# Performance work log

Measured on AMD Instinct MI355X. Metric: run time of the kernel, lower is better.

Reference implementation:

```python
import jax, jax.numpy as jnp
import numpy as np

CH, H, N, N_SSM, SEQ_L = 1, 1024, 64, 1024, 2048


def setup_inputs() -> dict:
    key = jax.random.key(0)
    ks = jax.random.split(key, 5)
    return {
        "C_ri": jax.random.normal(ks[0], (CH, H, N, 2), dtype=jnp.float32),
        "log_dt": jax.random.normal(ks[1], (H,), dtype=jnp.float32),
        "B_ri": jax.random.normal(ks[2], (N_SSM, N, 2), dtype=jnp.float32),
        "inv_A_real": jax.random.normal(ks[3], (N_SSM, N), dtype=jnp.float32),
        "A_imag": jax.random.normal(ks[4], (N_SSM, N), dtype=jnp.float32),
        "L": SEQ_L,
    }


def _kernel(C_ri, log_dt, B_ri, inv_A_real, A_imag, L):
    # Reconstruct complex params from real views (torch view_as_complex)
    C = C_ri[..., 0] + 1j * C_ri[..., 1]        # (CH, H, N) complex64
    B = B_ri[..., 0] + 1j * B_ri[..., 1]        # (n_ssm, N)
    A = -jnp.exp(inv_A_real) + 1j * A_imag      # (n_ssm, N), Re(A) < 0

    rep = log_dt.shape[0] // inv_A_real.shape[0]  # H // n_ssm
    B = jnp.tile(B, (rep, 1))                   # 't n -> (v t) n' : (H, N)
    A = jnp.tile(A, (rep, 1))                   # (H, N)

    dt = jnp.exp(log_dt)                        # (H,), rate = 1.0
    dtA = A * dt[:, None]                       # (H, N)

    # C <- B * C * dt / (1 - dtA/2)   (bilinear discretization of input/output)
    Ct = (B[None] * C) / (1.0 - dtA / 2) * dt[:, None]   # (CH, H, N)
    dA = (1.0 + dtA / 2) / (1.0 - dtA / 2)      # (H, N), |dA| < 1
    dA_log = jnp.log(dA)                        # (H, N)

    # log-Vandermonde: K[c,h,l] = 2 * Re( sum_n Ct[c,h,n] * exp(dA_log[h,n] * l) )
    l = jnp.arange(L, dtype=jnp.float32)
    V = jnp.exp(dA_log[:, :, None] * l)         # (H, N, L) complex
    K = 2.0 * jnp.einsum('chn,hnl->chl', Ct, V).real  # (CH, H, L)
    return K


def reference(C_ri, log_dt, B_ri, inv_A_real, A_imag, L):
    # state=None path: returns (K, K_state=None); we return K
    return _kernel(C_ri, log_dt, B_ri, inv_A_real, A_imag, L)
```

## Files before the change

kernel.cpp:

```cpp
#include <hip/hip_runtime.h>
#include <math.h>

#define CH 1
#define H 1024
#define NN 64
#define N_SSM 1024
#define SEQ_L 2048
#define TPB 128
#define LPT 16

typedef float v2f __attribute__((ext_vector_type(2)));

__device__ __forceinline__ v2f lo2(const float4 f) { v2f r; r.x = f.x; r.y = f.y; return r; }
__device__ __forceinline__ v2f hi2(const float4 f) { v2f r; r.x = f.z; r.y = f.w; return r; }

__global__ __launch_bounds__(TPB) void sskd_kernel(
    const float* __restrict__ C_ri, const float* __restrict__ log_dt,
    const float* __restrict__ B_ri, const float* __restrict__ inv_A_real,
    const float* __restrict__ A_imag, float* __restrict__ out)
{
    const int h   = blockIdx.x;
    const int tid = threadIdx.x;

    __shared__ __align__(16) float4 sU1[8][33], sV1[8][33], sU8[8][33], sV8[8][33];
    __shared__ __align__(16) float4 sT[16][33];
    __shared__ __align__(16) float4 sPQ[32];
    __shared__ double sW8r[NN], sW8i[NN], sW16r[NN], sW16i[NN], sW256r[NN], sW256i[NN];
    __shared__ double sCtr[NN], sCti[NN], sCdr[NN], sCdi[NN];

    if (tid < NN) {
        const int n = tid;
        const double dt = exp((double)log_dt[h]);
        const double Ar = -exp((double)inv_A_real[h * NN + n]);
        const double Ai = (double)A_imag[h * NN + n];
        const double hr = 0.5 * Ar * dt, hi = 0.5 * Ai * dt;
        const double den_r = 1.0 - hr, den_i = -hi;
        const double num_r = 1.0 + hr, num_i = hi;
        const double inv_den = 1.0 / (den_r * den_r + den_i * den_i);
        const double dAr = (num_r * den_r + num_i * den_i) * inv_den;
        const double dAi = (num_i * den_r - num_r * den_i) * inv_den;
        const int    bh = h % N_SSM;
        const double Br = B_ri[(bh * NN + n) * 2 + 0];
        const double Bi = B_ri[(bh * NN + n) * 2 + 1];
        const double Cr = C_ri[(h * NN + n) * 2 + 0];
        const double Ci = C_ri[(h * NN + n) * 2 + 1];
        const double BCr = Br * Cr - Bi * Ci;
        const double BCi = Br * Ci + Bi * Cr;
        const double sc = 2.0 * dt * inv_den;
        const double ctr = (BCr * den_r + BCi * den_i) * sc;
        const double cti = (BCi * den_r - BCr * den_i) * sc;
        sCtr[n] = ctr; sCti[n] = cti;
        sCdr[n] = ctr * dAr - cti * dAi;
        sCdi[n] = ctr * dAi + cti * dAr;
        float* pqp = (float*)&sPQ[n >> 1];
        pqp[(n & 1)]     = (float)(2.0 * dAr);
        pqp[2 + (n & 1)] = (float)(dAr * dAr + dAi * dAi);
        double wr = dAr, wi = dAi, tr;
        tr = wr * wr - wi * wi; wi = 2.0 * wr * wi; wr = tr;
        tr = wr * wr - wi * wi; wi = 2.0 * wr * wi; wr = tr;
        tr = wr * wr - wi * wi; wi = 2.0 * wr * wi; wr = tr;
        sW8r[n] = wr; sW8i[n] = wi;
        tr = wr * wr - wi * wi; wi = 2.0 * wr * wi; wr = tr;
        sW16r[n] = wr; sW16i[n] = wi;
        tr = wr * wr - wi * wi; wi = 2.0 * wr * wi; wr = tr;
        tr = wr * wr - wi * wi; wi = 2.0 * wr * wi; wr = tr;
        tr = wr * wr - wi * wi; wi = 2.0 * wr * wi; wr = tr;
        tr = wr * wr - wi * wi; wi = 2.0 * wr * wi; wr = tr;
        sW256r[n] = wr; sW256i[n] = wi;
    }
    __syncthreads();

    {
        const int n = tid & 63;
        const int g = tid >> 6;
        const int np = n >> 1, nc = n & 1;
        {
            const double ur = sW16r[n], ui = sW16i[n];
            double Vr = 1.0, Vi = 0.0;
            if (g) {
                double ar = ur, ai = ui, t;
                t = ar * ar - ai * ai; ai = 2.0 * ar * ai; ar = t;
                t = ar * ar - ai * ai; ai = 2.0 * ar * ai; ar = t;
                t = ar * ar - ai * ai; ai = 2.0 * ar * ai; ar = t;
                Vr = ar; Vi = ai;
            }
            #pragma unroll
            for (int i = 0; i < 8; ++i) {
                float* bp = (float*)&sT[8 * g + i][np];
                bp[nc] = (float)Vr; bp[2 + nc] = (float)Vi;
                const double t = Vr * ur - Vi * ui; Vi = Vr * ui + Vi * ur; Vr = t;
            }
        }
        {
            const double wr = sW256r[n], wi = sW256i[n];
            const double er = sW8r[n],  ei = sW8i[n];
            const double ctr = sCtr[n], cti = sCti[n];
            const double cdr = sCdr[n], cdi = sCdi[n];
            double Wr = 1.0, Wi = 0.0;
            if (g) {
                double ar = wr, ai = wi, t;
                t = ar * ar - ai * ai; ai = 2.0 * ar * ai; ar = t;
                t = ar * ar - ai * ai; ai = 2.0 * ar * ai; ar = t;
                Wr = ar; Wi = ai;
            }
            #pragma unroll
            for (int i = 0; i < 4; ++i) {
                const int t1 = 4 * g + i;
                const double u1r = ctr * Wr - cti * Wi, u1i = ctr * Wi + cti * Wr;
                const double v1r = cdr * Wr - cdi * Wi, v1i = cdr * Wi + cdi * Wr;
                const double u8r = u1r * er - u1i * ei, u8i = u1r * ei + u1i * er;
                const double v8r = v1r * er - v1i * ei, v8i = v1r * ei + v1i * er;
                float* a = (float*)&sU1[t1][np]; a[nc] = (float)u1r; a[2 + nc] = (float)u1i;
                float* b = (float*)&sV1[t1][np]; b[nc] = (float)v1r; b[2 + nc] = (float)v1i;
                float* c = (float*)&sU8[t1][np]; c[nc] = (float)u8r; c[2 + nc] = (float)u8i;
                float* d = (float*)&sV8[t1][np]; d[nc] = (float)v8r; d[2 + nc] = (float)v8i;
                const double t = Wr * wr - Wi * wi; Wi = Wr * wi + Wi * wr; Wr = t;
            }
        }
    }
    __syncthreads();

    const int t1 = tid >> 4;
    const int t0 = tid & 15;

    v2f acc[LPT];
    #pragma unroll
    for (int k = 0; k < LPT; ++k) acc[k] = (v2f)(0.0f);

    float4 u1 = sU1[t1][0], v1 = sV1[t1][0], u8 = sU8[t1][0], v8 = sV8[t1][0];
    float4 tt = sT[t0][0],  pq = sPQ[0];

    #pragma unroll 2
    for (int m = 0; m < NN / 2; ++m) {
        const int mn = (m + 1) & 31;
        const float4 u1n = sU1[t1][mn], v1n = sV1[t1][mn];
        const float4 u8n = sU8[t1][mn], v8n = sV8[t1][mn];
        const float4 ttn = sT[t0][mn],  pqn = sPQ[mn];

        const v2f br = lo2(tt), bi = hi2(tt);
        const v2f p  = lo2(pq), q  = hi2(pq);

        v2f xA2 = lo2(u1) * br - hi2(u1) * bi;
        v2f xA1 = lo2(v1) * br - hi2(v1) * bi;
        v2f xB2 = lo2(u8) * br - hi2(u8) * bi;
        v2f xB1 = lo2(v8) * br - hi2(v8) * bi;
        acc[0] += xA2; acc[1] += xA1;
        acc[8] += xB2; acc[9] += xB1;
        #pragma unroll
        for (int k = 2; k < 8; ++k) {
            const v2f xn = p * xA1 - q * xA2;
            acc[k] += xn;     xA2 = xA1; xA1 = xn;
            const v2f yn = p * xB1 - q * xB2;
            acc[8 + k] += yn; xB2 = xB1; xB1 = yn;
        }

        u1 = u1n; v1 = v1n; u8 = u8n; v8 = v8n; tt = ttn; pq = pqn;
    }

    float4 o;
    float4* op = (float4*)(out + (size_t)h * SEQ_L + tid * LPT);
    o.x = acc[0].x  + acc[0].y;  o.y = acc[1].x  + acc[1].y;
    o.z = acc[2].x  + acc[2].y;  o.w = acc[3].x  + acc[3].y;
    op[0] = o;
    o.x = acc[4].x  + acc[4].y;  o.y = acc[5].x  + acc[5].y;
    o.z = acc[6].x  + acc[6].y;  o.w = acc[7].x  + acc[7].y;
    op[1] = o;
    o.x = acc[8].x  + acc[8].y;  o.y = acc[9].x  + acc[9].y;
    o.z = acc[10].x + acc[10].y; o.w = acc[11].x + acc[11].y;
    op[2] = o;
    o.x = acc[12].x + acc[12].y; o.y = acc[13].x + acc[13].y;
    o.z = acc[14].x + acc[14].y; o.w = acc[15].x + acc[15].y;
    op[3] = o;
}

extern "C" void kernel_launch(void* const* d_in, const int* in_sizes, int n_in,
                              void* d_out, int out_size, void* d_ws, size_t ws_size,
                              hipStream_t stream) {
    const float* C_ri       = (const float*)d_in[0];
    const float* log_dt     = (const float*)d_in[1];
    const float* B_ri       = (const float*)d_in[2];
    const float* inv_A_real = (const float*)d_in[3];
    const float* A_imag     = (const float*)d_in[4];
    float* out = (float*)d_out;

    sskd_kernel<<<dim3(H), dim3(TPB), 0, stream>>>(
        C_ri, log_dt, B_ri, inv_A_real, A_imag, out);
}
```

Measured before the change: 75.18 us.

## Split mode sum across 4 lanes with DPP reduction, use 512 threads per block

Raises the block to 512 threads and partitions the 32 mode pairs into 4 slices per output group, so each thread runs a single 16-step Chebyshev-style recurrence over 8 mode pairs. Partial sums are then combined across lanes with DPP quad swaps. The precomputed tables shrink: the separate U8/V8 tables go away and the power tables are built with binary exponentiation per group. This adds parallelism and latency hiding per head at the cost of cross-lane reduction and a longer serial recurrence chain, which may affect fp32 accuracy.

```diff
diff --git a/kernel.cpp b/kernel.cpp
--- a/kernel.cpp
+++ b/kernel.cpp
@@ -6,13 +6,24 @@
 #define NN 64
 #define N_SSM 1024
 #define SEQ_L 2048
-#define TPB 128
+#define TPB 512
 #define LPT 16
+#define NSLICE 4
+#define MPT 8
 
 typedef float v2f __attribute__((ext_vector_type(2)));
 
-__device__ __forceinline__ v2f lo2(const float4 f) { v2f r; r.x = f.x; r.y = f.y; return r; }
-__device__ __forceinline__ v2f hi2(const float4 f) { v2f r; r.x = f.z; r.y = f.w; return r; }
+static __device__ __forceinline__ v2f lo2(const float4 f){ v2f r; r.x=f.x; r.y=f.y; return r; }
+static __device__ __forceinline__ v2f hi2(const float4 f){ v2f r; r.x=f.z; r.y=f.w; return r; }
+
+static __device__ __forceinline__ float qswap1(float x){
+    return __builtin_bit_cast(float,
+        __builtin_amdgcn_mov_dpp(__builtin_bit_cast(int,x), 0xB1, 0xF, 0xF, true));
+}
+static __device__ __forceinline__ float qswap2(float x){
+    return __builtin_bit_cast(float,
+        __builtin_amdgcn_mov_dpp(__builtin_bit_cast(int,x), 0x4E, 0xF, 0xF, true));
+}
 
 __global__ __launch_bounds__(TPB) void sskd_kernel(
     const float* __restrict__ C_ri, const float* __restrict__ log_dt,
@@ -22,11 +33,9 @@
     const int h   = blockIdx.x;
     const int tid = threadIdx.x;
 
-    __shared__ __align__(16) float4 sU1[8][33], sV1[8][33], sU8[8][33], sV8[8][33];
-    __shared__ __align__(16) float4 sT[16][33];
-    __shared__ __align__(16) float4 sPQ[32];
-    __shared__ double sW8r[NN], sW8i[NN], sW16r[NN], sW16i[NN], sW256r[NN], sW256i[NN];
-    __shared__ double sCtr[NN], sCti[NN], sCdr[NN], sCdi[NN];
+    __shared__ __align__(16) float4 sU1[8][33], sV1[8][33], sT[16][33], sPQ[32];
+    __shared__ double dW16r[NN], dW16i[NN], dW256r[NN], dW256i[NN],
+                      dCtr[NN],  dCti[NN],  dCdr[NN],  dCdi[NN];
 
     if (tid < NN) {
         const int n = tid;
@@ -35,10 +44,9 @@
         const double Ai = (double)A_imag[h * NN + n];
         const double hr = 0.5 * Ar * dt, hi = 0.5 * Ai * dt;
         const double den_r = 1.0 - hr, den_i = -hi;
-        const double num_r = 1.0 + hr, num_i = hi;
         const double inv_den = 1.0 / (den_r * den_r + den_i * den_i);
-        const double dAr = (num_r * den_r + num_i * den_i) * inv_den;
-        const double dAi = (num_i * den_r - num_r * den_i) * inv_den;
+        const double dAr = ((1.0 + hr) * den_r + hi * den_i) * inv_den;
+        const double dAi = (hi * den_r - (1.0 + hr) * den_i) * inv_den;
         const int    bh = h % N_SSM;
         const double Br = B_ri[(bh * NN + n) * 2 + 0];
         const double Bi = B_ri[(bh * NN + n) * 2 + 1];
@@ -49,24 +57,23 @@
         const double sc = 2.0 * dt * inv_den;
         const double ctr = (BCr * den_r + BCi * den_i) * sc;
         const double cti = (BCi * den_r - BCr * den_i) * sc;
-        sCtr[n] = ctr; sCti[n] = cti;
-        sCdr[n] = ctr * dAr - cti * dAi;
-        sCdi[n] = ctr * dAi + cti * dAr;
+        dCtr[n] = ctr; dCti[n] = cti;
+        dCdr[n] = ctr * dAr - cti * dAi;
+        dCdi[n] = ctr * dAi + cti * dAr;
         float* pqp = (float*)&sPQ[n >> 1];
         pqp[(n & 1)]     = (float)(2.0 * dAr);
         pqp[2 + (n & 1)] = (float)(dAr * dAr + dAi * dAi);
         double wr = dAr, wi = dAi, tr;
-        tr = wr * wr - wi * wi; wi = 2.0 * wr * wi; wr = tr;
-        tr = wr * wr - wi * wi; wi = 2.0 * wr * wi; wr = tr;
-        tr = wr * wr - wi * wi; wi = 2.0 * wr * wi; wr = tr;
-        sW8r[n] = wr; sW8i[n] = wi;
-        tr = wr * wr - wi * wi; wi = 2.0 * wr * wi; wr = tr;
-        sW16r[n] = wr; sW16i[n] = wi;
-        tr = wr * wr - wi * wi; wi = 2.0 * wr * wi; wr = tr;
-        tr = wr * wr - wi * wi; wi = 2.0 * wr * wi; wr = tr;
-        tr = wr * wr - wi * wi; wi = 2.0 * wr * wi; wr = tr;
-        tr = wr * wr - wi * wi; wi = 2.0 * wr * wi; wr = tr;
-        sW256r[n] = wr; sW256i[n] = wi;
+        tr = wr*wr - wi*wi; wi = 2.0*wr*wi; wr = tr;
+        tr = wr*wr - wi*wi; wi = 2.0*wr*wi; wr = tr;
+        tr = wr*wr - wi*wi; wi = 2.0*wr*wi; wr = tr;
+        tr = wr*wr - wi*wi; wi = 2.0*wr*wi; wr = tr;
+        dW16r[n] = wr; dW16i[n] = wi;
+        tr = wr*wr - wi*wi; wi = 2.0*wr*wi; wr = tr;
+        tr = wr*wr - wi*wi; wi = 2.0*wr*wi; wr = tr;
+        tr = wr*wr - wi*wi; wi = 2.0*wr*wi; wr = tr;
+        tr = wr*wr - wi*wi; wi = 2.0*wr*wi; wr = tr;
+        dW256r[n] = wr; dW256i[n] = wi;
     }
     __syncthreads();
 
@@ -75,102 +82,84 @@
         const int g = tid >> 6;
         const int np = n >> 1, nc = n & 1;
         {
-            const double ur = sW16r[n], ui = sW16i[n];
+            const double ur = dW16r[n], ui = dW16i[n];
+            const double a2r = ur*ur - ui*ui,     a2i = 2.0*ur*ui;
+            const double a4r = a2r*a2r - a2i*a2i, a4i = 2.0*a2r*a2i;
             double Vr = 1.0, Vi = 0.0;
-            if (g) {
-                double ar = ur, ai = ui, t;
-                t = ar * ar - ai * ai; ai = 2.0 * ar * ai; ar = t;
-                t = ar * ar - ai * ai; ai = 2.0 * ar * ai; ar = t;
-                t = ar * ar - ai * ai; ai = 2.0 * ar * ai; ar = t;
-                Vr = ar; Vi = ai;
-            }
+            if (g & 1) { Vr = a2r; Vi = a2i; }
+            if (g & 2) { const double t = Vr*a4r - Vi*a4i; Vi = Vr*a4i + Vi*a4r; Vr = t; }
+            if (g & 4) { const double a8r = a4r*a4r - a4i*a4i, a8i = 2.0*a4r*a4i;
+                         const double t = Vr*a8r - Vi*a8i; Vi = Vr*a8i + Vi*a8r; Vr = t; }
             #pragma unroll
-            for (int i = 0; i < 8; ++i) {
-                float* bp = (float*)&sT[8 * g + i][np];
+            for (int i = 0; i < 2; ++i) {
+                float* bp = (float*)&sT[2*g + i][np];
                 bp[nc] = (float)Vr; bp[2 + nc] = (float)Vi;
-                const double t = Vr * ur - Vi * ui; Vi = Vr * ui + Vi * ur; Vr = t;
+                const double t = Vr*ur - Vi*ui; Vi = Vr*ui + Vi*ur; Vr = t;
             }
         }
         {
-            const double wr = sW256r[n], wi = sW256i[n];
-            const double er = sW8r[n],  ei = sW8i[n];
-            const double ctr = sCtr[n], cti = sCti[n];
-            const double cdr = sCdr[n], cdi = sCdi[n];
+            const double wr = dW256r[n], wi = dW256i[n];
+            const double b2r = wr*wr - wi*wi,     b2i = 2.0*wr*wi;
+            const double b4r = b2r*b2r - b2i*b2i, b4i = 2.0*b2r*b2i;
             double Wr = 1.0, Wi = 0.0;
-            if (g) {
-                double ar = wr, ai = wi, t;
-                t = ar * ar - ai * ai; ai = 2.0 * ar * ai; ar = t;
-                t = ar * ar - ai * ai; ai = 2.0 * ar * ai; ar = t;
-                Wr = ar; Wi = ai;
-            }
-            #pragma unroll
-            for (int i = 0; i < 4; ++i) {
-                const int t1 = 4 * g + i;
-                const double u1r = ctr * Wr - cti * Wi, u1i = ctr * Wi + cti * Wr;
-                const double v1r = cdr * Wr - cdi * Wi, v1i = cdr * Wi + cdi * Wr;
-                const double u8r = u1r * er - u1i * ei, u8i = u1r * ei + u1i * er;
-                const double v8r = v1r * er - v1i * ei, v8i = v1r * ei + v1i * er;
-                float* a = (float*)&sU1[t1][np]; a[nc] = (float)u1r; a[2 + nc] = (float)u1i;
-                float* b = (float*)&sV1[t1][np]; b[nc] = (float)v1r; b[2 + nc] = (float)v1i;
-                float* c = (float*)&sU8[t1][np]; c[nc] = (float)u8r; c[2 + nc] = (float)u8i;
-                float* d = (float*)&sV8[t1][np]; d[nc] = (float)v8r; d[2 + nc] = (float)v8i;
-                const double t = Wr * wr - Wi * wi; Wi = Wr * wi + Wi * wr; Wr = t;
-            }
+            if (g & 1) { Wr = wr; Wi = wi; }
+            if (g & 2) { const double t = Wr*b2r - Wi*b2i; Wi = Wr*b2i + Wi*b2r; Wr = t; }
+            if (g & 4) { const double t = Wr*b4r - Wi*b4i; Wi = Wr*b4i + Wi*b4r; Wr = t; }
+            const double ctr = dCtr[n], cti = dCti[n], cdr = dCdr[n], cdi = dCdi[n];
+            float* a = (float*)&sU1[g][np];
+            a[nc] = (float)(ctr*Wr - cti*Wi); a[2 + nc] = (float)(ctr*Wi + cti*Wr);
+            float* b = (float*)&sV1[g][np];
+            b[nc] = (float)(cdr*Wr - cdi*Wi); b[2 + nc] = (float)(cdr*Wi + cdi*Wr);
         }
     }
     __syncthreads();
 
-    const int t1 = tid >> 4;
-    const int t0 = tid & 15;
+    const int s  = tid & 3;
+    const int u0 = (tid >> 2) & 15;
+    const int w  = tid >> 6;
 
     v2f acc[LPT];
     #pragma unroll
     for (int k = 0; k < LPT; ++k) acc[k] = (v2f)(0.0f);
 
-    float4 u1 = sU1[t1][0], v1 = sV1[t1][0], u8 = sU8[t1][0], v8 = sV8[t1][0];
-    float4 tt = sT[t0][0],  pq = sPQ[0];
+    const int M0 = MPT * s;
+    #pragma unroll 2
+    for (int j = 0; j < MPT; ++j) {
+        const int m = M0 + j;
+        const float4 A  = sU1[w][m];
+        const float4 Bv = sV1[w][m];
+        const float4 Tt = sT[u0][m];
+        const float4 Pq = sPQ[m];
+        const v2f br = lo2(Tt), bi = hi2(Tt);
+        const v2f p  = lo2(Pq), qq = hi2(Pq);
 
-    #pragma unroll 2
-    for (int m = 0; m < NN / 2; ++m) {
-        const int mn = (m + 1) & 31;
-        const float4 u1n = sU1[t1][mn], v1n = sV1[t1][mn];
-        const float4 u8n = sU8[t1][mn], v8n = sV8[t1][mn];
-        const float4 ttn = sT[t0][mn],  pqn = sPQ[mn];
+        v2f x2 = lo2(A)  * br - hi2(A)  * bi;
+        v2f x1 = lo2(Bv) * br - hi2(Bv) * bi;
+        acc[0] += x2; acc[1] += x1;
+        #pragma unroll
+        for (int k = 2; k < LPT; ++k) {
+            const v2f xn = p * x1 - qq * x2;
+            acc[k] += xn;
+            x2 = x1; x1 = xn;
+        }
+    }
 
-        const v2f br = lo2(tt), bi = hi2(tt);
-        const v2f p  = lo2(pq), q  = hi2(pq);
-
-        v2f xA2 = lo2(u1) * br - hi2(u1) * bi;
-        v2f xA1 = lo2(v1) * br - hi2(v1) * bi;
-        v2f xB2 = lo2(u8) * br - hi2(u8) * bi;
-        v2f xB1 = lo2(v8) * br - hi2(v8) * bi;
-        acc[0] += xA2; acc[1] += xA1;
-        acc[8] += xB2; acc[9] += xB1;
-        #pragma unroll
-        for (int k = 2; k < 8; ++k) {
-            const v2f xn = p * xA1 - q * xA2;
-            acc[k] += xn;     xA2 = xA1; xA1 = xn;
-            const v2f yn = p * xB1 - q * xB2;
-            acc[8 + k] += yn; xB2 = xB1; xB1 = yn;
-        }
-
-        u1 = u1n; v1 = v1n; u8 = u8n; v8 = v8n; tt = ttn; pq = pqn;
+    float r[LPT];
+    #pragma unroll
+    for (int k = 0; k < LPT; ++k) {
+        float v = acc[k].x + acc[k].y;
+        v += qswap1(v);
+        v += qswap2(v);
+        r[k] = v;
     }
 
     float4 o;
-    float4* op = (float4*)(out + (size_t)h * SEQ_L + tid * LPT);
-    o.x = acc[0].x  + acc[0].y;  o.y = acc[1].x  + acc[1].y;
-    o.z = acc[2].x  + acc[2].y;  o.w = acc[3].x  + acc[3].y;
-    op[0] = o;
-    o.x = acc[4].x  + acc[4].y;  o.y = acc[5].x  + acc[5].y;
-    o.z = acc[6].x  + acc[6].y;  o.w = acc[7].x  + acc[7].y;
-    op[1] = o;
-    o.x = acc[8].x  + acc[8].y;  o.y = acc[9].x  + acc[9].y;
-    o.z = acc[10].x + acc[10].y; o.w = acc[11].x + acc[11].y;
-    op[2] = o;
-    o.x = acc[12].x + acc[12].y; o.y = acc[13].x + acc[13].y;
-    o.z = acc[14].x + acc[14].y; o.w = acc[15].x + acc[15].y;
-    op[3] = o;
+    if      (s == 0) { o.x = r[0];  o.y = r[1];  o.z = r[2];  o.w = r[3];  }
+    else if (s == 1) { o.x = r[4];  o.y = r[5];  o.z = r[6];  o.w = r[7];  }
+    else if (s == 2) { o.x = r[8];  o.y = r[9];  o.z = r[10]; o.w = r[11]; }
+    else             { o.x = r[12]; o.y = r[13]; o.z = r[14]; o.w = r[15]; }
+    const int u = tid >> 2;
+    *(float4*)(out + (size_t)h * SEQ_L + u * LPT + 4 * s) = o;
 }
 
 extern "C" void kernel_launch(void* const* d_in, const int* in_sizes, int n_in,
```

Result: no change. 74.64 us (-0.7%).
